# Performance work log

Hardware: AMD Instinct MI355X
Metric: run time of the kernel (lower is better)

Reference implementation:

```python
import jax, jax.numpy as jnp
import numpy as np

B = 1024
INPUT_SIZE = 2048
OUTPUT_SIZE = 2048
E = 131072  # number of sparse connections


def setup_inputs() -> dict:
    key = jax.random.key(0)
    k1, k2, k3, k4 = jax.random.split(key, 4)
    x = jax.random.normal(k1, (B, INPUT_SIZE), dtype=jnp.float32)
    weights = jax.random.normal(k2, (E,), dtype=jnp.float32)
    in_idx = jax.random.randint(k3, (E,), 0, INPUT_SIZE, dtype=jnp.int64)
    out_idx = jax.random.randint(k4, (E,), 0, OUTPUT_SIZE, dtype=jnp.int64)
    return {"x": x, "weights": weights, "in_idx": in_idx, "out_idx": out_idx}


def reference(x, weights, in_idx, out_idx):
    # Original: for (i, o), w in connections: output[:, o] += w * x[:, i]
    # Vectorized as a single gather-multiply-scatter (duplicates sum):
    contrib = x[:, in_idx] * weights[None, :]  # [B, E]
    out = jnp.zeros((x.shape[0], OUTPUT_SIZE), dtype=x.dtype)
    out = out.at[:, out_idx].add(contrib)  # scatter-add along output dim
    return out
```

## Files before the change

### kernel.cpp

```cpp
#include <hip/hip_runtime.h>

#define BATCH  1024
#define IN_SZ  2048
#define OUT_SZ 2048
#define E_N    131072

#define NT     256
#define KMAX   128
#define CH     8
#define CPAD   16
#define FBLK   128
#define TBLK   512
#define PBASE  0xAAAAAAAAu

__device__ __forceinline__ unsigned int bf16_rne(float f) {
    unsigned int u = __float_as_uint(f);
    return (u + 0x7FFFu + ((u >> 16) & 1u)) >> 16;
}

__global__ __launch_bounds__(NT) void prep_kernel(
    const float* __restrict__ x,
    const int4* __restrict__ iidx4, const int4* __restrict__ oidx4,
    const float4* __restrict__ w4,
    unsigned short* __restrict__ xt, int* __restrict__ cursor,
    unsigned int* __restrict__ ell) {
    const int tid = threadIdx.x;
    const int b   = blockIdx.x;

    if (b < FBLK) {
        const int q = b * NT + tid;
        const int4   ii = iidx4[q];
        const int4   oo = oidx4[q];
        const float4 ww = w4[q];
        #pragma unroll
        for (int j = 0; j < 4; ++j) {
            const int i = (&ii.x)[j];
            const int o = (&oo.x)[j];
            const unsigned int packed = (bf16_rne((&ww.x)[j]) << 16) | (unsigned int)i;
            const int raw = atomicAdd(&cursor[o * CPAD], 1);
            const unsigned int kp = (unsigned int)raw - PBASE;
            const unsigned int slot = kp < KMAX ? kp : (unsigned int)raw;
            if (slot < KMAX)
                ell[(size_t)o * KMAX + slot] = packed;
        }
    } else {
        __shared__ float lds[64][65];
        const int bt = b - FBLK;
        const int jj = bt & 7, kk = bt >> 3;
        const int r0 = ((((jj >> 2) << 3) | (kk & 7))) * 64;
        const int c0 = ((((kk >> 3) << 2) | (jj & 3))) * 64;
        #pragma unroll
        for (int k = 0; k < 16; ++k) {
            const int idx = k * NT + tid;
            lds[idx >> 6][idx & 63] =
                x[(size_t)(r0 + (idx >> 6)) * IN_SZ + c0 + (idx & 63)];
        }
        __syncthreads();
        #pragma unroll
        for (int k = 0; k < 8; ++k) {
            const int idx = k * NT + tid;
            const int cl = idx >> 5;
            const int rp = (idx & 31) * 2;
            const unsigned int v =
                bf16_rne(lds[rp][cl]) | (bf16_rne(lds[rp + 1][cl]) << 16);
            *(unsigned int*)&xt[(size_t)(c0 + cl) * BATCH + r0 + rp] = v;
        }
    }
}

__global__ __launch_bounds__(NT) void spmm6_kernel(
    const unsigned short* __restrict__ xt, const unsigned int* __restrict__ ell,
    const int* __restrict__ cursor, float* __restrict__ out) {
    __shared__ float tile[4][516];
    const int tid  = threadIdx.x;
    const int wv_  = tid >> 6;
    const int lane = tid & 63;
    const int b    = blockIdx.x;
    const int half = (b >> 2) & 1;
    const int r0   = half * 512;
    const int c0   = (((b >> 3) << 2) | (b & 3)) * 4;
    const int cs   = __builtin_amdgcn_readfirstlane(c0 + wv_);

    const int raw = cursor[cs * CPAD];
    const unsigned int ud = (unsigned int)raw - PBASE;
    int cnt = (ud < 256u) ? (int)ud : raw;
    cnt = cnt < 0 ? 0 : (cnt > KMAX ? KMAX : cnt);
    const int nch = (cnt + CH - 1) / CH;
    const unsigned int* ep = ell + (size_t)cs * KMAX;
    const unsigned short* xtb = xt + r0 + lane * 8;

    float a[8];
    #pragma unroll
    for (int k = 0; k < 8; ++k) a[k] = 0.f;

    if (nch > 0) {
        unsigned int e0[CH], e1[CH];
        #pragma unroll
        for (int j = 0; j < CH; ++j) e0[j] = ep[j];
        for (int g = 0; g < nch; ++g) {
            const int gn = (g + 1 < nch) ? g + 1 : g;
            #pragma unroll
            for (int j = 0; j < CH; ++j) e1[j] = ep[gn * CH + j];
            uint4 xv[CH];
            #pragma unroll
            for (int j = 0; j < CH; ++j)
                xv[j] = *(const uint4*)(xtb + ((size_t)(e0[j] & 0x7FFu) << 10));
            #pragma unroll
            for (int j = 0; j < CH; ++j) {
                const float wv = __uint_as_float(e0[j] & 0xFFFF0000u);
                a[0] = fmaf(wv, __uint_as_float(xv[j].x << 16),         a[0]);
                a[1] = fmaf(wv, __uint_as_float(xv[j].x & 0xFFFF0000u), a[1]);
                a[2] = fmaf(wv, __uint_as_float(xv[j].y << 16),         a[2]);
                a[3] = fmaf(wv, __uint_as_float(xv[j].y & 0xFFFF0000u), a[3]);
                a[4] = fmaf(wv, __uint_as_float(xv[j].z << 16),         a[4]);
                a[5] = fmaf(wv, __uint_as_float(xv[j].z & 0xFFFF0000u), a[5]);
                a[6] = fmaf(wv, __uint_as_float(xv[j].w << 16),         a[6]);
                a[7] = fmaf(wv, __uint_as_float(xv[j].w & 0xFFFF0000u), a[7]);
            }
            #pragma unroll
            for (int j = 0; j < CH; ++j) e0[j] = e1[j];
        }
    }

    *(float4*)&tile[wv_][lane * 8]     = make_float4(a[0], a[1], a[2], a[3]);
    *(float4*)&tile[wv_][lane * 8 + 4] = make_float4(a[4], a[5], a[6], a[7]);
    __syncthreads();

    #pragma unroll
    for (int h = 0; h < 512; h += NT) {
        const int row = h + tid;
        float* op = out + (size_t)(r0 + row) * OUT_SZ + c0;
        *(float4*)op = make_float4(tile[0][row], tile[1][row],
                                   tile[2][row], tile[3][row]);
    }
}

__global__ __launch_bounds__(NT) void sparse_row_kernel(
    const float* __restrict__ x, const float* __restrict__ w,
    const int* __restrict__ iidx, const int* __restrict__ oidx,
    float* __restrict__ out) {
    __shared__ float xs[IN_SZ];
    __shared__ float acc[OUT_SZ];
    const int b = blockIdx.x, tid = threadIdx.x;
    const float4* xrow = (const float4*)(x + (size_t)b * IN_SZ);
    float4* xs4 = (float4*)xs;
    for (int t = tid; t < IN_SZ / 4; t += NT) xs4[t] = xrow[t];
    float4* acc4 = (float4*)acc;
    const float4 z = make_float4(0.f, 0.f, 0.f, 0.f);
    for (int t = tid; t < OUT_SZ / 4; t += NT) acc4[t] = z;
    __syncthreads();
    for (int e = tid; e < E_N; e += NT)
        atomicAdd(&acc[oidx[e]], w[e] * xs[iidx[e]]);
    __syncthreads();
    float4* orow = (float4*)(out + (size_t)b * OUT_SZ);
    for (int t = tid; t < OUT_SZ / 4; t += NT) orow[t] = acc4[t];
}

extern "C" void kernel_launch(void* const* d_in, const int* in_sizes, int n_in,
                              void* d_out, int out_size, void* d_ws, size_t ws_size,
                              hipStream_t stream) {
    const float* x    = (const float*)d_in[0];
    const float* wts  = (const float*)d_in[1];
    const int*   iidx = (const int*)d_in[2];
    const int*   oidx = (const int*)d_in[3];
    float* out = (float*)d_out;
    (void)in_sizes; (void)n_in; (void)out_size;

    const size_t cursor_bytes = (size_t)OUT_SZ * CPAD * sizeof(int);
    const size_t ell_bytes    = (size_t)OUT_SZ * KMAX * sizeof(unsigned int);
    const size_t xt_bytes     = (size_t)IN_SZ * BATCH * sizeof(unsigned short);
    if (ws_size < cursor_bytes + ell_bytes + xt_bytes) {
        sparse_row_kernel<<<BATCH, NT, 0, stream>>>(x, wts, iidx, oidx, out);
        return;
    }

    int* cursor = (int*)d_ws;
    unsigned int*   ell = (unsigned int*)((char*)d_ws + cursor_bytes);
    unsigned short* xt  = (unsigned short*)((char*)d_ws + cursor_bytes + ell_bytes);

    prep_kernel<<<FBLK + TBLK, NT, 0, stream>>>(x, (const int4*)iidx,
                                                (const int4*)oidx, (const float4*)wts,
                                                xt, cursor, ell);
    spmm6_kernel<<<1024, NT, 0, stream>>>(xt, ell, cursor, out);
}
```

Measured before the change: 88.99 us.

## Replicate transposed bf16 x per XCD-group and use nontemporal loads/stores

The prep kernel now writes eight copies of the transposed bf16 x, one per block-index residue (likely the XCD that block is dispatched to). Each copy holds only the half of the batch that the matching spmm blocks read, so every XCD gathers from its own L2-local copy instead of sharing one array. The x reads in prep and the output stores in spmm become nontemporal. The cost is four times more transpose blocks and four times more xt bytes written and held in workspace.

```diff
diff --git a/kernel.cpp b/kernel.cpp
--- a/kernel.cpp
+++ b/kernel.cpp
@@ -10,8 +10,11 @@
 #define CH     8
 #define CPAD   16
 #define FBLK   128
-#define TBLK   512
+#define TGBLK  2048
 #define PBASE  0xAAAAAAAAu
+#define XT_COPY (IN_SZ * 512)
+
+typedef float  __attribute__((ext_vector_type(4))) floatx4;
 
 __device__ __forceinline__ unsigned int bf16_rne(float f) {
     unsigned int u = __float_as_uint(f);
@@ -46,14 +49,20 @@
     } else {
         __shared__ float lds[64][65];
         const int bt = b - FBLK;
-        const int jj = bt & 7, kk = bt >> 3;
-        const int r0 = ((((jj >> 2) << 3) | (kk & 7))) * 64;
-        const int c0 = ((((kk >> 3) << 2) | (jj & 3))) * 64;
+        const int g  = bt & 7;
+        const int kk = bt >> 3;
+        const int ct = kk >> 3;
+        const int rt = kk & 7;
+        const int c0 = ct * 64;
+        const int r0g = (g >> 2) * 512 + rt * 64;
+        unsigned short* xtc = xt + (size_t)g * XT_COPY;
+
         #pragma unroll
         for (int k = 0; k < 16; ++k) {
             const int idx = k * NT + tid;
-            lds[idx >> 6][idx & 63] =
-                x[(size_t)(r0 + (idx >> 6)) * IN_SZ + c0 + (idx & 63)];
+            const int r = idx >> 6, cl = idx & 63;
+            lds[r][cl] = __builtin_nontemporal_load(
+                &x[(size_t)(r0g + r) * IN_SZ + c0 + cl]);
         }
         __syncthreads();
         #pragma unroll
@@ -63,12 +72,12 @@
             const int rp = (idx & 31) * 2;
             const unsigned int v =
                 bf16_rne(lds[rp][cl]) | (bf16_rne(lds[rp + 1][cl]) << 16);
-            *(unsigned int*)&xt[(size_t)(c0 + cl) * BATCH + r0 + rp] = v;
+            *(unsigned int*)&xtc[(size_t)(c0 + cl) * 512 + rt * 64 + rp] = v;
         }
     }
 }
 
-__global__ __launch_bounds__(NT) void spmm6_kernel(
+__global__ __launch_bounds__(NT) void spmm7_kernel(
     const unsigned short* __restrict__ xt, const unsigned int* __restrict__ ell,
     const int* __restrict__ cursor, float* __restrict__ out) {
     __shared__ float tile[4][516];
@@ -76,9 +85,11 @@
     const int wv_  = tid >> 6;
     const int lane = tid & 63;
     const int b    = blockIdx.x;
-    const int half = (b >> 2) & 1;
+    const int g    = b & 7;
+    const int half = g >> 2;
     const int r0   = half * 512;
-    const int c0   = (((b >> 3) << 2) | (b & 3)) * 4;
+    const int cg   = ((b >> 3) << 2) | (g & 3);
+    const int c0   = cg * 4;
     const int cs   = __builtin_amdgcn_readfirstlane(c0 + wv_);
 
     const int raw = cursor[cs * CPAD];
@@ -87,7 +98,7 @@
     cnt = cnt < 0 ? 0 : (cnt > KMAX ? KMAX : cnt);
     const int nch = (cnt + CH - 1) / CH;
     const unsigned int* ep = ell + (size_t)cs * KMAX;
-    const unsigned short* xtb = xt + r0 + lane * 8;
+    const unsigned short* xtb = xt + (size_t)g * XT_COPY + lane * 8;
 
     float a[8];
     #pragma unroll
@@ -97,14 +108,14 @@
         unsigned int e0[CH], e1[CH];
         #pragma unroll
         for (int j = 0; j < CH; ++j) e0[j] = ep[j];
-        for (int g = 0; g < nch; ++g) {
-            const int gn = (g + 1 < nch) ? g + 1 : g;
+        for (int gch = 0; gch < nch; ++gch) {
+            const int gn = (gch + 1 < nch) ? gch + 1 : gch;
             #pragma unroll
             for (int j = 0; j < CH; ++j) e1[j] = ep[gn * CH + j];
             uint4 xv[CH];
             #pragma unroll
             for (int j = 0; j < CH; ++j)
-                xv[j] = *(const uint4*)(xtb + ((size_t)(e0[j] & 0x7FFu) << 10));
+                xv[j] = *(const uint4*)(xtb + ((size_t)(e0[j] & 0x7FFu) << 9));
             #pragma unroll
             for (int j = 0; j < CH; ++j) {
                 const float wv = __uint_as_float(e0[j] & 0xFFFF0000u);
@@ -129,9 +140,11 @@
     #pragma unroll
     for (int h = 0; h < 512; h += NT) {
         const int row = h + tid;
-        float* op = out + (size_t)(r0 + row) * OUT_SZ + c0;
-        *(float4*)op = make_float4(tile[0][row], tile[1][row],
-                                   tile[2][row], tile[3][row]);
+        floatx4* op = (floatx4*)(out + (size_t)(r0 + row) * OUT_SZ + c0);
+        floatx4 v;
+        v.x = tile[0][row]; v.y = tile[1][row];
+        v.z = tile[2][row]; v.w = tile[3][row];
+        __builtin_nontemporal_store(v, op);
     }
 }
 
@@ -168,7 +181,7 @@
 
     const size_t cursor_bytes = (size_t)OUT_SZ * CPAD * sizeof(int);
     const size_t ell_bytes    = (size_t)OUT_SZ * KMAX * sizeof(unsigned int);
-    const size_t xt_bytes     = (size_t)IN_SZ * BATCH * sizeof(unsigned short);
+    const size_t xt_bytes     = (size_t)8 * XT_COPY * sizeof(unsigned short);
     if (ws_size < cursor_bytes + ell_bytes + xt_bytes) {
         sparse_row_kernel<<<BATCH, NT, 0, stream>>>(x, wts, iidx, oidx, out);
         return;
@@ -178,8 +191,8 @@
     unsigned int*   ell = (unsigned int*)((char*)d_ws + cursor_bytes);
     unsigned short* xt  = (unsigned short*)((char*)d_ws + cursor_bytes + ell_bytes);
 
-    prep_kernel<<<FBLK + TBLK, NT, 0, stream>>>(x, (const int4*)iidx,
-                                                (const int4*)oidx, (const float4*)wts,
-                                                xt, cursor, ell);
-    spmm6_kernel<<<1024, NT, 0, stream>>>(xt, ell, cursor, out);
+    prep_kernel<<<FBLK + TGBLK, NT, 0, stream>>>(x, (const int4*)iidx,
+                                                 (const int4*)oidx, (const float4*)wts,
+                                                 xt, cursor, ell);
+    spmm7_kernel<<<1024, NT, 0, stream>>>(xt, ell, cursor, out);
 }
```

Result: slower. 112.4 us (+26.3%).
